# Kernel tuning notes

Hardware: AMD Instinct MI355X
Metric: run time of the kernel (lower is better)

The kernel has to match this reference:

```python
import jax, jax.numpy as jnp
import numpy as np

D = 1024        # d_model
H = 16          # query heads
HKV = 4         # kv heads (GQA)
HD = D // H     # head dim = 64
MAX_T = 1024
EPS = 1e-6
CAP = 50.0      # logit softcap


def _rope_cache(max_t, hd):
    inv = 1.0 / (10000.0 ** (np.arange(0, hd, 2, dtype=np.float32) / hd))  # (hd/2,)
    t = np.arange(max_t, dtype=np.float32)
    f = np.outer(t, inv)                                                   # (max_t, hd/2)
    return jnp.asarray(np.cos(f)), jnp.asarray(np.sin(f))


def setup_inputs() -> dict:
    key = jax.random.key(0)
    ks = jax.random.split(key, 5)
    x = jax.random.normal(ks[0], (2, 64, 256, D), jnp.float32)  # (B,T,S,D)
    wq = jax.random.normal(ks[1], (D, H * HD), jnp.float32) * 0.02
    wk = jax.random.normal(ks[2], (D, HKV * HD), jnp.float32) * 0.02
    wv = jax.random.normal(ks[3], (D, HKV * HD), jnp.float32) * 0.02
    wo = jax.random.normal(ks[4], (H * HD, D), jnp.float32) * 0.02
    q_scale = jnp.ones((HD,), jnp.float32)  # QKNorm learnable gains
    k_scale = jnp.ones((HD,), jnp.float32)
    rope_cos, rope_sin = _rope_cache(MAX_T, HD)
    return {"x": x, "wq": wq, "wk": wk, "wv": wv, "wo": wo,
            "q_scale": q_scale, "k_scale": k_scale,
            "rope_cos": rope_cos, "rope_sin": rope_sin}


def _rmsnorm(v, scale):
    return v * jax.lax.rsqrt(jnp.mean(v * v, axis=-1, keepdims=True) + EPS) * scale


def reference(x, wq, wk, wv, wo, q_scale, k_scale, rope_cos, rope_sin):
    B, T, S, Dm = x.shape
    # fold spatial positions into batch: each position attends causally over time
    xt = x.transpose(0, 2, 1, 3).reshape(B * S, T, Dm)          # (N,T,D)
    q = (xt @ wq).reshape(B * S, T, H, HD)
    k = (xt @ wk).reshape(B * S, T, HKV, HD)
    v = (xt @ wv).reshape(B * S, T, HKV, HD)
    # QK-norm (RMSNorm over head_dim) before RoPE
    q = _rmsnorm(q, q_scale)
    k = _rmsnorm(k, k_scale)
    # 1D RoPE over temporal positions (split-half convention)
    cos = rope_cos[:T][None, :, None, :]                        # (1,T,1,HD/2)
    sin = rope_sin[:T][None, :, None, :]

    def rot(u):
        u1, u2 = jnp.split(u, 2, axis=-1)
        return jnp.concatenate([u1 * cos - u2 * sin, u1 * sin + u2 * cos], axis=-1)

    q = rot(q)
    k = rot(k)
    # GQA: expand kv heads to match query heads
    rep = H // HKV
    k = jnp.repeat(k, rep, axis=2)
    v = jnp.repeat(v, rep, axis=2)
    scores = jnp.einsum('nthd,nshd->nhts', q, k) / np.float32(np.sqrt(HD))
    scores = CAP * jnp.tanh(scores / CAP)                        # logit softcap
    causal = jnp.tril(jnp.ones((T, T), bool))
    scores = jnp.where(causal, scores, jnp.float32(-1e30))
    a = jax.nn.softmax(scores, axis=-1)
    o = jnp.einsum('nhts,nshd->nthd', a, v).reshape(B * S, T, H * HD) @ wo
    return o.reshape(B, S, T, Dm).transpose(0, 2, 1, 3)          # (B,T,S,D)
```

## Files before the change

### kernel.cpp

```cpp
#include <hip/hip_runtime.h>

#define DM   1024
#define NHQ  16
#define NKVH 4
#define HDIM 64
#define TTT  64
#define SSS  256
#define NBB  2
#define MROWS 32768

using short8 = __attribute__((ext_vector_type(8))) short;
using f32x4  = __attribute__((ext_vector_type(4))) float;

__device__ __forceinline__ short f2bf(float f) {
  union { float f; unsigned u; } v; v.f = f;
  unsigned r = v.u + 0x7fffu + ((v.u >> 16) & 1u);
  return (short)(r >> 16);
}

__device__ __forceinline__ f32x4 mfma16(short8 a, short8 b, f32x4 c) {
  return __builtin_amdgcn_mfma_f32_16x16x32_bf16(a, b, c, 0, 0, 0);
}

__device__ __forceinline__ void gload_lds16(const void* g, void* l) {
  __builtin_amdgcn_global_load_lds(
      (const __attribute__((address_space(1))) void*)g,
      (__attribute__((address_space(3))) void*)l, 16, 0, 0);
}

__global__ __launch_bounds__(256) void k_xconv(const float* __restrict__ x,
                                               short* __restrict__ xb) {
  int r = blockIdx.x;
  int n = r >> 6, t = r & 63;
  int b = n >> 8, s = n & 255;
  const float4* src = (const float4*)(x + ((size_t)((b * TTT + t) * SSS + s)) * DM);
  short4* dst = (short4*)(xb + (size_t)r * DM);
  float4 v = src[threadIdx.x];
  short4 o;
  o.x = f2bf(v.x); o.y = f2bf(v.y); o.z = f2bf(v.z); o.w = f2bf(v.w);
  dst[threadIdx.x] = o;
}

__global__ __launch_bounds__(256) void k_wt(const float* __restrict__ w,
                                            short* __restrict__ wt, int cols) {
  __shared__ float tile[32][33];
  int ctiles = cols >> 5;
  int tj = blockIdx.x % ctiles;
  int td = blockIdx.x / ctiles;
  int lx = threadIdx.x & 31, ly = threadIdx.x >> 5;
  #pragma unroll
  for (int rr = 0; rr < 32; rr += 8)
    tile[rr + ly][lx] = w[(size_t)(td * 32 + rr + ly) * cols + tj * 32 + lx];
  __syncthreads();
  #pragma unroll
  for (int rr = 0; rr < 32; rr += 8)
    wt[(size_t)(tj * 32 + rr + ly) * 1024 + td * 32 + lx] = f2bf(tile[lx][rr + ly]);
}

#define GEMM256_8PH(Ab, Bb)                                                    \
  const int tid = threadIdx.x, lane = tid & 63, wid = tid >> 6;                \
  const int wr = wid >> 2, wc = wid & 3;                                       \
  const int ln15 = lane & 15, lhi = lane >> 4;                                 \
  const int rsw = ln15 & 7;                                                    \
  f32x4 acc[8][4] = {};                                                        \
  auto SHALF = [&](const short* gb, short* lb, int half, int kt) {             \
    _Pragma("unroll")                                                          \
    for (int i = 0; i < 2; ++i) {                                              \
      int c = i * 512 + tid;                                                   \
      int row = c >> 3, slot = c & 7;                                          \
      gload_lds16(gb + (size_t)(half * 128 + row) * 1024 + kt                  \
                     + ((slot ^ (row & 7)) << 3),                              \
                  lb + half * 8192 + c * 8);                                   \
    }                                                                          \
  };                                                                           \
                        \
  SHALF(Ab, sm, 0, 0); SHALF(Ab, sm, 1, 0);                                    \
  SHALF(Bb, sm + 16384, 0, 0); SHALF(Bb, sm + 16384, 1, 0);                    \
  SHALF(Ab, sm + 32768, 0, 64); SHALF(Ab, sm + 32768, 1, 64);                  \
  SHALF(Bb, sm + 49152, 0, 64); SHALF(Bb, sm + 49152, 1, 64);                  \
  asm volatile("s_waitcnt vmcnt(8)" ::: "memory");                             \
  __builtin_amdgcn_s_barrier();                                                \
  for (int g = 0; g < 16; ++g) {                                               \
    short* cA = sm + (g & 1) * 32768;                                          \
    short* cB = cA + 16384;                                                    \
    short* nA = sm + ((g + 1) & 1) * 32768;                                    \
    const bool iA = (g > 0) && (g < 15);                                       \
    const bool iB = (g < 14);                                                  \
    short8 a[4], b0[4], b1[4];                                                 \
                       \
    _Pragma("unroll")                                                          \
    for (int n = 0; n < 4; ++n)                                                \
      b0[n] = *(const short8*)(cB + (wc * 64 + n * 16 + ln15) * 64             \
                                  + ((lhi ^ rsw) << 3));                       \
    _Pragma("unroll")                                                          \
    for (int m = 0; m < 4; ++m)                                                \
      a[m] = *(const short8*)(cA + (wr * 128 + m * 16 + ln15) * 64             \
                                 + ((lhi ^ rsw) << 3));                        \
    if (iA) SHALF(Ab, nA, 0, (g + 1) * 64);                                    \
    __builtin_amdgcn_s_barrier();                                              \
    asm volatile("s_waitcnt lgkmcnt(0)" ::: "memory");                         \
    __builtin_amdgcn_s_setprio(1);                                             \
    _Pragma("unroll")                                                          \
    for (int m = 0; m < 4; ++m)                                                \
      _Pragma("unroll")                                                        \
      for (int n = 0; n < 4; ++n) acc[m][n] = mfma16(a[m], b0[n], acc[m][n]);  \
    __builtin_amdgcn_s_setprio(0);                                             \
    __builtin_amdgcn_s_barrier();                                              \
                               \
    _Pragma("unroll")                                                          \
    for (int m = 0; m < 4; ++m)                                                \
      a[m] = *(const short8*)(cA + (wr * 128 + 64 + m * 16 + ln15) * 64        \
                                 + ((lhi ^ rsw) << 3));                        \
    if (iA) SHALF(Ab, nA, 1, (g + 1) * 64);                                    \
    __builtin_amdgcn_s_barrier();                                              \
    asm volatile("s_waitcnt lgkmcnt(0)" ::: "memory");                         \
    __builtin_amdgcn_s_setprio(1);                                             \
    _Pragma("unroll")                                                          \
    for (int m = 0; m < 4; ++m)                                                \
      _Pragma("unroll")                                                        \
      for (int n = 0; n < 4; ++n)                                              \
        acc[4 + m][n] = mfma16(a[m], b0[n], acc[4 + m][n]);                    \
    __builtin_amdgcn_s_setprio(0);                                             \
    __builtin_amdgcn_s_barrier();                                              \
                                        \
    _Pragma("unroll")                                                          \
    for (int n = 0; n < 4; ++n)                                                \
      b1[n] = *(const short8*)(cB + (wc * 64 + n * 16 + ln15) * 64             \
                                  + (((4 + lhi) ^ rsw) << 3));                 \
    _Pragma("unroll")                                                          \
    for (int m = 0; m < 4; ++m)                                                \
      a[m] = *(const short8*)(cA + (wr * 128 + m * 16 + ln15) * 64             \
                                 + (((4 + lhi) ^ rsw) << 3));                  \
    __builtin_amdgcn_s_barrier();                                              \
    asm volatile("s_waitcnt lgkmcnt(0)" ::: "memory");                         \
    __builtin_amdgcn_s_setprio(1);                                             \
    _Pragma("unroll")                                                          \
    for (int m = 0; m < 4; ++m)                                                \
      _Pragma("unroll")                                                        \
      for (int n = 0; n < 4; ++n) acc[m][n] = mfma16(a[m], b1[n], acc[m][n]);  \
    __builtin_amdgcn_s_setprio(0);                                             \
    __builtin_amdgcn_s_barrier();                                              \
                  \
    _Pragma("unroll")                                                          \
    for (int m = 0; m < 4; ++m)                                                \
      a[m] = *(const short8*)(cA + (wr * 128 + 64 + m * 16 + ln15) * 64        \
                                 + (((4 + lhi) ^ rsw) << 3));                  \
    if (iB) { SHALF(Bb, cB, 0, (g + 2) * 64); SHALF(Bb, cB, 1, (g + 2) * 64); }\
    __builtin_amdgcn_s_barrier();                                              \
    asm volatile("s_waitcnt lgkmcnt(0)" ::: "memory");                         \
    __builtin_amdgcn_s_setprio(1);                                             \
    _Pragma("unroll")                                                          \
    for (int m = 0; m < 4; ++m)                                                \
      _Pragma("unroll")                                                        \
      for (int n = 0; n < 4; ++n)                                              \
        acc[4 + m][n] = mfma16(a[m], b1[n], acc[4 + m][n]);                    \
    __builtin_amdgcn_s_setprio(0);                                             \
    if (g < 14)       asm volatile("s_waitcnt vmcnt(4)" ::: "memory");         \
    else if (g == 14) asm volatile("s_waitcnt vmcnt(0)" ::: "memory");         \
    __builtin_amdgcn_s_barrier();                                              \
  }

__global__ __launch_bounds__(512, 2) void k_qkv(
    const short* __restrict__ xb, const short* __restrict__ wt,
    const float* __restrict__ qscale, const float* __restrict__ kscale,
    const float* __restrict__ rcos, const float* __restrict__ rsin,
    short* __restrict__ qb, short* __restrict__ kb, short* __restrict__ vb) {
  __shared__ __align__(16) short sm[65536];
  const int bid = blockIdx.x;
  const int swz = (bid & 7) * 96 + (bid >> 3);
  const int tn = swz % 6, tm = swz / 6;
  const short* Ab = xb + (size_t)tm * 256 * 1024;
  const short* Bb = wt + (size_t)tn * 256 * 1024;
  GEMM256_8PH(Ab, Bb)

  short* ot = sm;
  if (tn < 5) {
    const float* scale = (tn < 4) ? qscale : kscale;
    float sc[4];
    #pragma unroll
    for (int n = 0; n < 4; ++n) sc[n] = scale[n * 16 + ln15];
    #pragma unroll
    for (int m = 0; m < 8; ++m) {
      #pragma unroll
      for (int j = 0; j < 4; ++j) {
        float ss = 0.f;
        #pragma unroll
        for (int n = 0; n < 4; ++n) { float v = acc[m][n][j]; ss += v * v; }
        #pragma unroll
        for (int off = 8; off; off >>= 1) ss += __shfl_xor(ss, off, 64);
        float rms = rsqrtf(ss * (1.f / 64.f) + 1e-6f);
        int rl = wr * 128 + m * 16 + lhi * 4 + j;
        int t = (tm * 256 + rl) & 63;
        #pragma unroll
        for (int n = 0; n < 2; ++n) {
          int i = n * 16 + ln15;
          float cs = rcos[t * 32 + i], sn = rsin[t * 32 + i];
          float v1 = acc[m][n][j] * rms * sc[n];
          float v2 = acc[m][n + 2][j] * rms * sc[n + 2];
          ot[rl * 256 + wc * 64 + i]      = f2bf(v1 * cs - v2 * sn);
          ot[rl * 256 + wc * 64 + i + 32] = f2bf(v1 * sn + v2 * cs);
        }
      }
    }
  } else {
    #pragma unroll
    for (int m = 0; m < 8; ++m)
      #pragma unroll
      for (int n = 0; n < 4; ++n)
        #pragma unroll
        for (int j = 0; j < 4; ++j) {
          int rl = wr * 128 + m * 16 + lhi * 4 + j;
          ot[rl * 256 + wc * 64 + n * 16 + ln15] = f2bf(acc[m][n][j]);
        }
  }
  __syncthreads();
  {
    int row = tid >> 1, half = tid & 1;
    int r = tm * 256 + row;
    const uint4* src = (const uint4*)(ot + row * 256 + half * 128);
    short* dst;
    if (tn < 4)       dst = qb + (size_t)r * 1024 + tn * 256 + half * 128;
    else if (tn == 4) dst = kb + (size_t)r * 256 + half * 128;
    else              dst = vb + (size_t)r * 256 + half * 128;
    uint4* d4 = (uint4*)dst;
    #pragma unroll
    for (int i = 0; i < 16; ++i) d4[i] = src[i];
  }
}

__global__ __launch_bounds__(256) void k_attn(const short* __restrict__ qb,
                                              const short* __restrict__ kb,
                                              const short* __restrict__ vb,
                                              short* __restrict__ ob) {
  __shared__ __align__(16) short Qs[64 * 72];
  __shared__ __align__(16) short Ks[64 * 72];
  __shared__ __align__(16) short Vt[64 * 72];
  __shared__ __align__(16) short Ps[64 * 72];
  int h = blockIdx.x & 15, n = blockIdx.x >> 4;
  int kvh = h >> 2;
  int tid = threadIdx.x, lane = tid & 63, wid = tid >> 6;
  for (int c = tid; c < 512; c += 256) {
    int row = c >> 3, c8 = c & 7;
    *(uint4*)(&Qs[row * 72 + c8 * 8]) =
        *(const uint4*)(qb + (size_t)(n * 64 + row) * 1024 + h * 64 + c8 * 8);
    *(uint4*)(&Ks[row * 72 + c8 * 8]) =
        *(const uint4*)(kb + (size_t)(n * 64 + row) * 256 + kvh * 64 + c8 * 8);
    short8 vv = *(const short8*)(vb + (size_t)(n * 64 + row) * 256 + kvh * 64 + c8 * 8);
    #pragma unroll
    for (int e = 0; e < 8; ++e) Vt[(c8 * 8 + e) * 72 + row] = vv[e];
  }
  __syncthreads();
  int ln15 = lane & 15, lhi = lane >> 4;
  f32x4 accs[4] = {};
  #pragma unroll
  for (int kk = 0; kk < 2; ++kk) {
    int ko = kk * 32 + lhi * 8;
    short8 aq = *(const short8*)(&Qs[(wid * 16 + ln15) * 72 + ko]);
    #pragma unroll
    for (int nn = 0; nn < 4; ++nn) {
      short8 bk = *(const short8*)(&Ks[(nn * 16 + ln15) * 72 + ko]);
      accs[nn] = mfma16(aq, bk, accs[nn]);
    }
  }
  int rowloc = wid * 16 + lhi * 4;
  float p[4][4];
  #pragma unroll
  for (int j = 0; j < 4; ++j) {
    int row = rowloc + j;
    float m = -3e38f;
    #pragma unroll
    for (int nn = 0; nn < 4; ++nn) {
      float s = accs[nn][j] * 0.125f;
      s = 50.f * tanhf(s * 0.02f);
      int col = nn * 16 + ln15;
      s = (col <= row) ? s : -1e30f;
      p[nn][j] = s;
      m = fmaxf(m, s);
    }
    #pragma unroll
    for (int off = 8; off; off >>= 1) m = fmaxf(m, __shfl_xor(m, off, 64));
    float sum = 0.f;
    #pragma unroll
    for (int nn = 0; nn < 4; ++nn) {
      float e = __expf(p[nn][j] - m);
      p[nn][j] = e; sum += e;
    }
    #pragma unroll
    for (int off = 8; off; off >>= 1) sum += __shfl_xor(sum, off, 64);
    float inv = 1.f / sum;
    #pragma unroll
    for (int nn = 0; nn < 4; ++nn) p[nn][j] *= inv;
  }
  #pragma unroll
  for (int nn = 0; nn < 4; ++nn)
    #pragma unroll
    for (int j = 0; j < 4; ++j)
      Ps[(rowloc + j) * 72 + nn * 16 + ln15] = f2bf(p[nn][j]);
  __syncthreads();
  f32x4 acco[4] = {};
  #pragma unroll
  for (int kk = 0; kk < 2; ++kk) {
    int ko = kk * 32 + lhi * 8;
    short8 ap = *(const short8*)(&Ps[(wid * 16 + ln15) * 72 + ko]);
    #pragma unroll
    for (int nn = 0; nn < 4; ++nn) {
      short8 bv = *(const short8*)(&Vt[(nn * 16 + ln15) * 72 + ko]);
      acco[nn] = mfma16(ap, bv, acco[nn]);
    }
  }
  #pragma unroll
  for (int nn = 0; nn < 4; ++nn)
    #pragma unroll
    for (int j = 0; j < 4; ++j) {
      int t = rowloc + j;
      ob[(size_t)(n * 64 + t) * 1024 + h * 64 + nn * 16 + ln15] = f2bf(acco[nn][j]);
    }
}

__global__ __launch_bounds__(512, 2) void k_out(const short* __restrict__ ab,
                                                const short* __restrict__ wt,
                                                float* __restrict__ out) {
  __shared__ __align__(16) short sm[65536];
  const int bid = blockIdx.x;
  const int swz = (bid & 7) * 64 + (bid >> 3);
  const int tn = swz & 3, tm = swz >> 2;
  const short* Ab = ab + (size_t)tm * 256 * 1024;
  const short* Bb = wt + (size_t)tn * 256 * 1024;
  GEMM256_8PH(Ab, Bb)

  float* of = (float*)sm;
  #pragma unroll
  for (int ch = 0; ch < 2; ++ch) {
    if (wr == ch) {
      #pragma unroll
      for (int m = 0; m < 8; ++m)
        #pragma unroll
        for (int n = 0; n < 4; ++n)
          #pragma unroll
          for (int j = 0; j < 4; ++j)
            of[(m * 16 + lhi * 4 + j) * 256 + wc * 64 + n * 16 + ln15] = acc[m][n][j];
    }
    __syncthreads();
    {
      int row = tid >> 2, q4 = tid & 3;
      int r = tm * 256 + ch * 128 + row;
      int nseq = r >> 6, t = r & 63;
      int b = nseq >> 8, s = nseq & 255;
      float* dst = out + ((size_t)((b * TTT + t) * SSS + s)) * DM + tn * 256 + q4 * 64;
      const float4* src = (const float4*)(of + row * 256 + q4 * 64);
      float4* d4 = (float4*)dst;
      #pragma unroll
      for (int i = 0; i < 16; ++i) d4[i] = src[i];
    }
    __syncthreads();
  }
}

extern "C" void kernel_launch(void* const* d_in, const int* in_sizes, int n_in,
                              void* d_out, int out_size, void* d_ws, size_t ws_size,
                              hipStream_t stream) {
  const float* x  = (const float*)d_in[0];
  const float* wq = (const float*)d_in[1];
  const float* wk = (const float*)d_in[2];
  const float* wv = (const float*)d_in[3];
  const float* wo = (const float*)d_in[4];
  const float* qs = (const float*)d_in[5];
  const float* ks = (const float*)d_in[6];
  const float* rc = (const float*)d_in[7];
  const float* rs = (const float*)d_in[8];
  float* out = (float*)d_out;
  char* ws = (char*)d_ws;

  short* xb    = (short*)(ws);
  short* wqkvT = (short*)(ws + 67108864);
  short* woT   = (short*)(ws + 70254592);
  short* qb    = (short*)(ws + 72351744);
  short* kb    = (short*)(ws + 139460608);
  short* vb    = (short*)(ws + 156237824);
  short* ob    = xb;

  k_xconv<<<MROWS, 256, 0, stream>>>(x, xb);
  k_wt<<<1024, 256, 0, stream>>>(wq, wqkvT, 1024);
  k_wt<<<256, 256, 0, stream>>>(wk, wqkvT + (size_t)1024 * 1024, 256);
  k_wt<<<256, 256, 0, stream>>>(wv, wqkvT + (size_t)1280 * 1024, 256);
  k_wt<<<1024, 256, 0, stream>>>(wo, woT, 1024);
  k_qkv<<<768, 512, 0, stream>>>(xb, wqkvT, qs, ks, rc, rs, qb, kb, vb);
  k_attn<<<512 * 16, 256, 0, stream>>>(qb, kb, vb, ob);
  k_out<<<512, 512, 0, stream>>>(ob, woT, out);
}
```

Baseline: 341.9 us.

## Fuse fp32-to-bf16 x conversion into QKV GEMM and restructure attention per sequence

The separate x conversion kernel is removed. The QKV GEMM now loads fp32 rows of x directly into registers, converts them to bf16 and writes them to LDS, replacing the async global-to-LDS path for the A operand. This drops a full write and reread of a 64 MB intermediate. Attention now runs one block per sequence, with each of 8 waves handling two heads. The tanh softcap is computed through exp and rcp, V is shared in LDS across heads, and the wider block size reduces launch count. The tradeoffs are more registers in the GEMM, which drops the minimum-occupancy hint of 2, and an A operand that is no longer async-loaded.

```diff
diff --git a/kernel.cpp b/kernel.cpp
--- a/kernel.cpp
+++ b/kernel.cpp
@@ -1,4 +1,5 @@
 #include <hip/hip_runtime.h>
+#include <hip/hip_bf16.h>
 
 #define DM   1024
 #define NHQ  16
@@ -10,12 +11,13 @@
 #define MROWS 32768
 
 using short8 = __attribute__((ext_vector_type(8))) short;
+using short4v = __attribute__((ext_vector_type(4))) short;
 using f32x4  = __attribute__((ext_vector_type(4))) float;
 
 __device__ __forceinline__ short f2bf(float f) {
-  union { float f; unsigned u; } v; v.f = f;
-  unsigned r = v.u + 0x7fffu + ((v.u >> 16) & 1u);
-  return (short)(r >> 16);
+  union { __hip_bfloat16 h; short s; } u;
+  u.h = __float2bfloat16(f);
+  return u.s;
 }
 
 __device__ __forceinline__ f32x4 mfma16(short8 a, short8 b, f32x4 c) {
@@ -26,19 +28,6 @@
   __builtin_amdgcn_global_load_lds(
       (const __attribute__((address_space(1))) void*)g,
       (__attribute__((address_space(3))) void*)l, 16, 0, 0);
-}
-
-__global__ __launch_bounds__(256) void k_xconv(const float* __restrict__ x,
-                                               short* __restrict__ xb) {
-  int r = blockIdx.x;
-  int n = r >> 6, t = r & 63;
-  int b = n >> 8, s = n & 255;
-  const float4* src = (const float4*)(x + ((size_t)((b * TTT + t) * SSS + s)) * DM);
-  short4* dst = (short4*)(xb + (size_t)r * DM);
-  float4 v = src[threadIdx.x];
-  short4 o;
-  o.x = f2bf(v.x); o.y = f2bf(v.y); o.z = f2bf(v.z); o.w = f2bf(v.w);
-  dst[threadIdx.x] = o;
 }
 
 __global__ __launch_bounds__(256) void k_wt(const float* __restrict__ w,
@@ -73,7 +62,6 @@
                   lb + half * 8192 + c * 8);                                   \
     }                                                                          \
   };                                                                           \
-                        \
   SHALF(Ab, sm, 0, 0); SHALF(Ab, sm, 1, 0);                                    \
   SHALF(Bb, sm + 16384, 0, 0); SHALF(Bb, sm + 16384, 1, 0);                    \
   SHALF(Ab, sm + 32768, 0, 64); SHALF(Ab, sm + 32768, 1, 64);                  \
@@ -87,7 +75,6 @@
     const bool iA = (g > 0) && (g < 15);                                       \
     const bool iB = (g < 14);                                                  \
     short8 a[4], b0[4], b1[4];                                                 \
-                       \
     _Pragma("unroll")                                                          \
     for (int n = 0; n < 4; ++n)                                                \
       b0[n] = *(const short8*)(cB + (wc * 64 + n * 16 + ln15) * 64             \
@@ -106,7 +93,6 @@
       for (int n = 0; n < 4; ++n) acc[m][n] = mfma16(a[m], b0[n], acc[m][n]);  \
     __builtin_amdgcn_s_setprio(0);                                             \
     __builtin_amdgcn_s_barrier();                                              \
-                               \
     _Pragma("unroll")                                                          \
     for (int m = 0; m < 4; ++m)                                                \
       a[m] = *(const short8*)(cA + (wr * 128 + 64 + m * 16 + ln15) * 64        \
@@ -122,7 +108,6 @@
         acc[4 + m][n] = mfma16(a[m], b0[n], acc[4 + m][n]);                    \
     __builtin_amdgcn_s_setprio(0);                                             \
     __builtin_amdgcn_s_barrier();                                              \
-                                        \
     _Pragma("unroll")                                                          \
     for (int n = 0; n < 4; ++n)                                                \
       b1[n] = *(const short8*)(cB + (wc * 64 + n * 16 + ln15) * 64             \
@@ -140,7 +125,6 @@
       for (int n = 0; n < 4; ++n) acc[m][n] = mfma16(a[m], b1[n], acc[m][n]);  \
     __builtin_amdgcn_s_setprio(0);                                             \
     __builtin_amdgcn_s_barrier();                                              \
-                  \
     _Pragma("unroll")                                                          \
     for (int m = 0; m < 4; ++m)                                                \
       a[m] = *(const short8*)(cA + (wr * 128 + 64 + m * 16 + ln15) * 64        \
@@ -160,8 +144,8 @@
     __builtin_amdgcn_s_barrier();                                              \
   }
 
-__global__ __launch_bounds__(512, 2) void k_qkv(
-    const short* __restrict__ xb, const short* __restrict__ wt,
+__global__ __launch_bounds__(512) void k_qkv(
+    const float* __restrict__ x, const short* __restrict__ wt,
     const float* __restrict__ qscale, const float* __restrict__ kscale,
     const float* __restrict__ rcos, const float* __restrict__ rsin,
     short* __restrict__ qb, short* __restrict__ kb, short* __restrict__ vb) {
@@ -169,9 +153,136 @@
   const int bid = blockIdx.x;
   const int swz = (bid & 7) * 96 + (bid >> 3);
   const int tn = swz % 6, tm = swz / 6;
-  const short* Ab = xb + (size_t)tm * 256 * 1024;
   const short* Bb = wt + (size_t)tn * 256 * 1024;
-  GEMM256_8PH(Ab, Bb)
+  const int tid = threadIdx.x, lane = tid & 63, wid = tid >> 6;
+  const int wr = wid >> 2, wc = wid & 3;
+  const int ln15 = lane & 15, lhi = lane >> 4;
+  const int rsw = ln15 & 7;
+  f32x4 acc[8][4] = {};
+  const int arow = tid >> 3, aslot = tid & 7;
+  const float* aptr[2][2];
+  #pragma unroll
+  for (int half = 0; half < 2; ++half)
+    #pragma unroll
+    for (int i = 0; i < 2; ++i) {
+      int row = half * 128 + i * 64 + arow;
+      int gr = tm * 256 + row;
+      int nseq = gr >> 6, t = gr & 63;
+      int b = nseq >> 8, s = nseq & 255;
+      aptr[half][i] = x + ((size_t)((b * 64 + t) * 256 + s)) * 1024
+                        + ((aslot ^ (row & 7)) << 3);
+    }
+  float4 ra[2][2][2], rb[2][2][2];
+  auto A_ISSUE = [&](float4 (&rg)[2][2][2], int half, int kt) {
+    #pragma unroll
+    for (int i = 0; i < 2; ++i) {
+      rg[half][i][0] = *(const float4*)(aptr[half][i] + kt);
+      rg[half][i][1] = *(const float4*)(aptr[half][i] + kt + 4);
+    }
+  };
+  auto A_WRITE = [&](float4 (&rg)[2][2][2], short* dA, int half) {
+    #pragma unroll
+    for (int i = 0; i < 2; ++i) {
+      short8 v;
+      #pragma unroll
+      for (int e = 0; e < 4; ++e) {
+        v[e]     = f2bf(rg[half][i][0][e]);
+        v[4 + e] = f2bf(rg[half][i][1][e]);
+      }
+      *(short8*)(dA + half * 8192 + (i * 512 + tid) * 8) = v;
+    }
+  };
+  auto BHALF = [&](short* lb, int half, int kt) {
+    #pragma unroll
+    for (int i = 0; i < 2; ++i) {
+      int c = i * 512 + tid;
+      int row = c >> 3, slot = c & 7;
+      gload_lds16(Bb + (size_t)(half * 128 + row) * 1024 + kt
+                     + ((slot ^ (row & 7)) << 3),
+                  lb + half * 8192 + c * 8);
+    }
+  };
+  A_ISSUE(ra, 0, 0); A_ISSUE(ra, 1, 0);
+  BHALF(sm + 16384, 0, 0); BHALF(sm + 16384, 1, 0);
+  A_ISSUE(rb, 0, 64); A_ISSUE(rb, 1, 64);
+  BHALF(sm + 49152, 0, 64); BHALF(sm + 49152, 1, 64);
+  asm volatile("s_waitcnt vmcnt(16)" ::: "memory");
+  A_WRITE(ra, sm, 0); A_WRITE(ra, sm, 1);
+  asm volatile("s_waitcnt vmcnt(4)" ::: "memory");
+  A_WRITE(rb, sm + 32768, 0); A_WRITE(rb, sm + 32768, 1);
+  asm volatile("s_waitcnt lgkmcnt(0)" ::: "memory");
+  __builtin_amdgcn_s_barrier();
+  for (int g = 0; g < 16; ++g) {
+    short* cA = sm + (g & 1) * 32768;
+    short* cB = cA + 16384;
+    short* nA = sm + ((g + 1) & 1) * 32768;
+    const bool iA = (g > 0) && (g < 15);
+    const bool iB = (g < 14);
+    short8 a[4], b0[4], b1[4];
+    #pragma unroll
+    for (int n = 0; n < 4; ++n)
+      b0[n] = *(const short8*)(cB + (wc * 64 + n * 16 + ln15) * 64 + ((lhi ^ rsw) << 3));
+    #pragma unroll
+    for (int m = 0; m < 4; ++m)
+      a[m] = *(const short8*)(cA + (wr * 128 + m * 16 + ln15) * 64 + ((lhi ^ rsw) << 3));
+    if (iA) A_ISSUE(ra, 0, (g + 1) * 64);
+    __builtin_amdgcn_s_barrier();
+    asm volatile("s_waitcnt lgkmcnt(0)" ::: "memory");
+    __builtin_amdgcn_s_setprio(1);
+    #pragma unroll
+    for (int m = 0; m < 4; ++m)
+      #pragma unroll
+      for (int n = 0; n < 4; ++n) acc[m][n] = mfma16(a[m], b0[n], acc[m][n]);
+    __builtin_amdgcn_s_setprio(0);
+    __builtin_amdgcn_s_barrier();
+    #pragma unroll
+    for (int m = 0; m < 4; ++m)
+      a[m] = *(const short8*)(cA + (wr * 128 + 64 + m * 16 + ln15) * 64 + ((lhi ^ rsw) << 3));
+    if (iA) A_ISSUE(ra, 1, (g + 1) * 64);
+    __builtin_amdgcn_s_barrier();
+    asm volatile("s_waitcnt lgkmcnt(0)" ::: "memory");
+    __builtin_amdgcn_s_setprio(1);
+    #pragma unroll
+    for (int m = 0; m < 4; ++m)
+      #pragma unroll
+      for (int n = 0; n < 4; ++n) acc[4 + m][n] = mfma16(a[m], b0[n], acc[4 + m][n]);
+    __builtin_amdgcn_s_setprio(0);
+    __builtin_amdgcn_s_barrier();
+    #pragma unroll
+    for (int n = 0; n < 4; ++n)
+      b1[n] = *(const short8*)(cB + (wc * 64 + n * 16 + ln15) * 64 + (((4 + lhi) ^ rsw) << 3));
+    #pragma unroll
+    for (int m = 0; m < 4; ++m)
+      a[m] = *(const short8*)(cA + (wr * 128 + m * 16 + ln15) * 64 + (((4 + lhi) ^ rsw) << 3));
+    if (iB) { BHALF(cB, 0, (g + 2) * 64); BHALF(cB, 1, (g + 2) * 64); }
+    __builtin_amdgcn_s_barrier();
+    asm volatile("s_waitcnt lgkmcnt(0)" ::: "memory");
+    __builtin_amdgcn_s_setprio(1);
+    #pragma unroll
+    for (int m = 0; m < 4; ++m)
+      #pragma unroll
+      for (int n = 0; n < 4; ++n) acc[m][n] = mfma16(a[m], b1[n], acc[m][n]);
+    __builtin_amdgcn_s_setprio(0);
+    __builtin_amdgcn_s_barrier();
+    #pragma unroll
+    for (int m = 0; m < 4; ++m)
+      a[m] = *(const short8*)(cA + (wr * 128 + 64 + m * 16 + ln15) * 64 + (((4 + lhi) ^ rsw) << 3));
+    __builtin_amdgcn_s_barrier();
+    asm volatile("s_waitcnt lgkmcnt(0)" ::: "memory");
+    __builtin_amdgcn_s_setprio(1);
+    #pragma unroll
+    for (int m = 0; m < 4; ++m)
+      #pragma unroll
+      for (int n = 0; n < 4; ++n) acc[4 + m][n] = mfma16(a[m], b1[n], acc[4 + m][n]);
+    __builtin_amdgcn_s_setprio(0);
+    if (g < 14)       asm volatile("s_waitcnt vmcnt(4)" ::: "memory");
+    else if (g == 14) asm volatile("s_waitcnt vmcnt(0)" ::: "memory");
+    if (iA) {
+      A_WRITE(ra, nA, 0); A_WRITE(ra, nA, 1);
+      asm volatile("s_waitcnt lgkmcnt(0)" ::: "memory");
+    }
+    __builtin_amdgcn_s_barrier();
+  }
 
   short* ot = sm;
   if (tn < 5) {
@@ -228,93 +339,127 @@
   }
 }
 
-__global__ __launch_bounds__(256) void k_attn(const short* __restrict__ qb,
+__global__ __launch_bounds__(512) void k_attn(const short* __restrict__ qb,
                                               const short* __restrict__ kb,
                                               const short* __restrict__ vb,
                                               short* __restrict__ ob) {
-  __shared__ __align__(16) short Qs[64 * 72];
-  __shared__ __align__(16) short Ks[64 * 72];
-  __shared__ __align__(16) short Vt[64 * 72];
-  __shared__ __align__(16) short Ps[64 * 72];
-  int h = blockIdx.x & 15, n = blockIdx.x >> 4;
-  int kvh = h >> 2;
-  int tid = threadIdx.x, lane = tid & 63, wid = tid >> 6;
-  for (int c = tid; c < 512; c += 256) {
-    int row = c >> 3, c8 = c & 7;
-    *(uint4*)(&Qs[row * 72 + c8 * 8]) =
-        *(const uint4*)(qb + (size_t)(n * 64 + row) * 1024 + h * 64 + c8 * 8);
-    *(uint4*)(&Ks[row * 72 + c8 * 8]) =
-        *(const uint4*)(kb + (size_t)(n * 64 + row) * 256 + kvh * 64 + c8 * 8);
-    short8 vv = *(const short8*)(vb + (size_t)(n * 64 + row) * 256 + kvh * 64 + c8 * 8);
-    #pragma unroll
-    for (int e = 0; e < 8; ++e) Vt[(c8 * 8 + e) * 72 + row] = vv[e];
+  __shared__ __align__(16) short Vt[256 * 72];
+  __shared__ __align__(16) short Ps[8][64 * 72];
+  const int n = blockIdx.x;
+  const int tid = threadIdx.x, lane = tid & 63, wid = tid >> 6;
+  const int ln15 = lane & 15, lhi = lane >> 4;
+  #pragma unroll
+  for (int it = 0; it < 4; ++it) {
+    int id = it * 512 + tid;
+    int s = id >> 5, c8 = id & 31;
+    short8 vv = *(const short8*)(vb + ((size_t)(n * 64 + s)) * 256 + c8 * 8);
+    #pragma unroll
+    for (int e = 0; e < 8; ++e) Vt[(c8 * 8 + e) * 72 + s] = vv[e];
   }
   __syncthreads();
-  int ln15 = lane & 15, lhi = lane >> 4;
-  f32x4 accs[4] = {};
+  short* Pt = &Ps[wid][0];
   #pragma unroll
-  for (int kk = 0; kk < 2; ++kk) {
-    int ko = kk * 32 + lhi * 8;
-    short8 aq = *(const short8*)(&Qs[(wid * 16 + ln15) * 72 + ko]);
+  for (int hh = 0; hh < 2; ++hh) {
+    const int h = wid + hh * 8;
+    const int kvh = h >> 2;
+    short8 bk[4][2], aq[4][2];
+    #pragma unroll
+    for (int m = 0; m < 4; ++m)
+      #pragma unroll
+      for (int kk = 0; kk < 2; ++kk)
+        bk[m][kk] = *(const short8*)(kb + ((size_t)(n * 64 + m * 16 + ln15)) * 256
+                                        + kvh * 64 + kk * 32 + lhi * 8);
+    #pragma unroll
+    for (int nn = 0; nn < 4; ++nn)
+      #pragma unroll
+      for (int kk = 0; kk < 2; ++kk)
+        aq[nn][kk] = *(const short8*)(qb + ((size_t)(n * 64 + nn * 16 + ln15)) * 1024
+                                         + h * 64 + kk * 32 + lhi * 8);
+    f32x4 sa[4][4] = {};
+    __builtin_amdgcn_s_setprio(1);
+    #pragma unroll
+    for (int kk = 0; kk < 2; ++kk)
+      #pragma unroll
+      for (int m = 0; m < 4; ++m)
+        #pragma unroll
+        for (int nn = 0; nn < 4; ++nn)
+          sa[m][nn] = mfma16(bk[m][kk], aq[nn][kk], sa[m][nn]);
+    __builtin_amdgcn_s_setprio(0);
+    #pragma unroll
+    for (int m = 0; m < 4; ++m)
+      #pragma unroll
+      for (int nn = 0; nn < 4; ++nn)
+        #pragma unroll
+        for (int j = 0; j < 4; ++j) {
+          float e2 = __expf(sa[m][nn][j] * 0.005f);
+          float cap = 50.f * (e2 - 1.f) * __builtin_amdgcn_rcpf(e2 + 1.f);
+          int scur = m * 16 + lhi * 4 + j, tcur = nn * 16 + ln15;
+          sa[m][nn][j] = (scur <= tcur) ? cap : -1e30f;
+        }
+    float inv[4];
     #pragma unroll
     for (int nn = 0; nn < 4; ++nn) {
-      short8 bk = *(const short8*)(&Ks[(nn * 16 + ln15) * 72 + ko]);
-      accs[nn] = mfma16(aq, bk, accs[nn]);
-    }
-  }
-  int rowloc = wid * 16 + lhi * 4;
-  float p[4][4];
-  #pragma unroll
-  for (int j = 0; j < 4; ++j) {
-    int row = rowloc + j;
-    float m = -3e38f;
-    #pragma unroll
-    for (int nn = 0; nn < 4; ++nn) {
-      float s = accs[nn][j] * 0.125f;
-      s = 50.f * tanhf(s * 0.02f);
-      int col = nn * 16 + ln15;
-      s = (col <= row) ? s : -1e30f;
-      p[nn][j] = s;
-      m = fmaxf(m, s);
-    }
-    #pragma unroll
-    for (int off = 8; off; off >>= 1) m = fmaxf(m, __shfl_xor(m, off, 64));
-    float sum = 0.f;
-    #pragma unroll
-    for (int nn = 0; nn < 4; ++nn) {
-      float e = __expf(p[nn][j] - m);
-      p[nn][j] = e; sum += e;
-    }
-    #pragma unroll
-    for (int off = 8; off; off >>= 1) sum += __shfl_xor(sum, off, 64);
-    float inv = 1.f / sum;
-    #pragma unroll
-    for (int nn = 0; nn < 4; ++nn) p[nn][j] *= inv;
-  }
-  #pragma unroll
-  for (int nn = 0; nn < 4; ++nn)
-    #pragma unroll
-    for (int j = 0; j < 4; ++j)
-      Ps[(rowloc + j) * 72 + nn * 16 + ln15] = f2bf(p[nn][j]);
-  __syncthreads();
-  f32x4 acco[4] = {};
-  #pragma unroll
-  for (int kk = 0; kk < 2; ++kk) {
-    int ko = kk * 32 + lhi * 8;
-    short8 ap = *(const short8*)(&Ps[(wid * 16 + ln15) * 72 + ko]);
-    #pragma unroll
-    for (int nn = 0; nn < 4; ++nn) {
-      short8 bv = *(const short8*)(&Vt[(nn * 16 + ln15) * 72 + ko]);
-      acco[nn] = mfma16(ap, bv, acco[nn]);
-    }
-  }
-  #pragma unroll
-  for (int nn = 0; nn < 4; ++nn)
-    #pragma unroll
-    for (int j = 0; j < 4; ++j) {
-      int t = rowloc + j;
-      ob[(size_t)(n * 64 + t) * 1024 + h * 64 + nn * 16 + ln15] = f2bf(acco[nn][j]);
-    }
+      float mx = -3e38f;
+      #pragma unroll
+      for (int m = 0; m < 4; ++m)
+        #pragma unroll
+        for (int j = 0; j < 4; ++j) mx = fmaxf(mx, sa[m][nn][j]);
+      mx = fmaxf(mx, __shfl_xor(mx, 16, 64));
+      mx = fmaxf(mx, __shfl_xor(mx, 32, 64));
+      float sum = 0.f;
+      #pragma unroll
+      for (int m = 0; m < 4; ++m)
+        #pragma unroll
+        for (int j = 0; j < 4; ++j) {
+          float e = __expf(sa[m][nn][j] - mx);
+          sa[m][nn][j] = e; sum += e;
+        }
+      sum += __shfl_xor(sum, 16, 64);
+      sum += __shfl_xor(sum, 32, 64);
+      inv[nn] = __builtin_amdgcn_rcpf(sum);
+    }
+    #pragma unroll
+    for (int nn = 0; nn < 4; ++nn)
+      #pragma unroll
+      for (int m = 0; m < 4; ++m) {
+        short4v w;
+        #pragma unroll
+        for (int j = 0; j < 4; ++j) w[j] = f2bf(sa[m][nn][j] * inv[nn]);
+        *(short4v*)(Pt + (nn * 16 + ln15) * 72 + m * 16 + lhi * 4) = w;
+      }
+    short8 ap[4][2], bv[4][2];
+    #pragma unroll
+    for (int m = 0; m < 4; ++m)
+      #pragma unroll
+      for (int kk = 0; kk < 2; ++kk)
+        ap[m][kk] = *(const short8*)(Pt + (m * 16 + ln15) * 72 + kk * 32 + lhi * 8);
+    #pragma unroll
+    for (int nn = 0; nn < 4; ++nn)
+      #pragma unroll
+      for (int kk = 0; kk < 2; ++kk)
+        bv[nn][kk] = *(const short8*)(&Vt[(kvh * 64 + nn * 16 + ln15) * 72 + kk * 32 + lhi * 8]);
+    f32x4 oa[4][4] = {};
+    __builtin_amdgcn_s_setprio(1);
+    #pragma unroll
+    for (int kk = 0; kk < 2; ++kk)
+      #pragma unroll
+      for (int m = 0; m < 4; ++m)
+        #pragma unroll
+        for (int nn = 0; nn < 4; ++nn)
+          oa[m][nn] = mfma16(ap[m][kk], bv[nn][kk], oa[m][nn]);
+    __builtin_amdgcn_s_setprio(0);
+    #pragma unroll
+    for (int m = 0; m < 4; ++m)
+      #pragma unroll
+      for (int nn = 0; nn < 4; ++nn)
+        #pragma unroll
+        for (int j = 0; j < 4; ++j)
+          Pt[(m * 16 + lhi * 4 + j) * 72 + nn * 16 + ln15] = f2bf(oa[m][nn][j]);
+    #pragma unroll
+    for (int c = 0; c < 8; ++c)
+      *(uint4*)(ob + ((size_t)(n * 64 + lane)) * 1024 + h * 64 + c * 8)
+          = *(const uint4*)(Pt + lane * 72 + c * 8);
+  }
 }
 
 __global__ __launch_bounds__(512, 2) void k_out(const short* __restrict__ ab,
@@ -371,20 +516,18 @@
   float* out = (float*)d_out;
   char* ws = (char*)d_ws;
 
-  short* xb    = (short*)(ws);
+  short* ob    = (short*)(ws);
   short* wqkvT = (short*)(ws + 67108864);
   short* woT   = (short*)(ws + 70254592);
   short* qb    = (short*)(ws + 72351744);
   short* kb    = (short*)(ws + 139460608);
   short* vb    = (short*)(ws + 156237824);
-  short* ob    = xb;
-
-  k_xconv<<<MROWS, 256, 0, stream>>>(x, xb);
+
   k_wt<<<1024, 256, 0, stream>>>(wq, wqkvT, 1024);
   k_wt<<<256, 256, 0, stream>>>(wk, wqkvT + (size_t)1024 * 1024, 256);
   k_wt<<<256, 256, 0, stream>>>(wv, wqkvT + (size_t)1280 * 1024, 256);
   k_wt<<<1024, 256, 0, stream>>>(wo, woT, 1024);
-  k_qkv<<<768, 512, 0, stream>>>(xb, wqkvT, qs, ks, rc, rs, qb, kb, vb);
-  k_attn<<<512 * 16, 256, 0, stream>>>(qb, kb, vb, ob);
+  k_qkv<<<768, 512, 0, stream>>>(x, wqkvT, qs, ks, rc, rs, qb, kb, vb);
+  k_attn<<<512, 512, 0, stream>>>(qb, kb, vb, ob);
   k_out<<<512, 512, 0, stream>>>(ob, woT, out);
 }
```

Result: slower. 356.8 us (+4.3%).
